# Kernel optimization log

Measured on AMD Instinct MI355X. Metric: run time of the kernel, lower is better.

Reference implementation:

```python
import jax, jax.numpy as jnp
import numpy as np

HEADS = 8

def setup_inputs() -> dict:
    key = jax.random.key(0)
    ks = jax.random.split(key, 5)
    B, C, H, W = 2, 256, 64, 64
    dim = C
    x = jax.random.normal(ks[0], (B, C, H, W), dtype=jnp.float32)
    # Linear weights stored as [in, out] so y = x @ W + b
    w_qkv = jax.random.normal(ks[1], (dim, 3 * dim), dtype=jnp.float32) * (dim ** -0.5)
    b_qkv = jax.random.normal(ks[2], (3 * dim,), dtype=jnp.float32) * 0.02
    w_out = jax.random.normal(ks[3], (dim, dim), dtype=jnp.float32) * (dim ** -0.5)
    b_out = jax.random.normal(ks[4], (dim,), dtype=jnp.float32) * 0.02
    return {"x": x, "w_qkv": w_qkv, "b_qkv": b_qkv, "w_out": w_out, "b_out": b_out}

def reference(x, w_qkv, b_qkv, w_out, b_out):
    B, C, H, W = x.shape
    h = HEADS
    d = C // h
    scale = d ** -0.5
    # [B, C, H, W] -> [B, N, C]
    tokens = x.reshape(B, C, H * W).transpose(0, 2, 1)
    qkv = tokens @ w_qkv + b_qkv  # [B, N, 3C]
    q, k, v = jnp.split(qkv, 3, axis=-1)
    def to_heads(t):
        Bn, N, _ = t.shape
        return t.reshape(Bn, N, h, d).transpose(0, 2, 1, 3)  # [B, h, N, d]
    q, k, v = map(to_heads, (q, k, v))
    dots = jnp.einsum('bhnd,bhmd->bhnm', q, k) * scale  # [B, h, N, N]
    attn = jax.nn.softmax(dots, axis=-1)
    out = jnp.einsum('bhnm,bhmd->bhnd', attn, v)  # [B, h, N, d]
    out = out.transpose(0, 2, 1, 3).reshape(B, H * W, C)  # [B, N, C]
    out = out @ w_out + b_out
    return out.transpose(0, 2, 1).reshape(B, C, H, W)
```

## Files before the change

### kernel.cpp

```cpp
#include <hip/hip_runtime.h>

typedef __attribute__((ext_vector_type(8))) short s16x8;
typedef __attribute__((ext_vector_type(4))) float f32x4;
typedef __attribute__((ext_vector_type(16))) float f32x16;
typedef __attribute__((ext_vector_type(2))) unsigned u32x2;
typedef __attribute__((ext_vector_type(4))) unsigned u32x4;

#define MFMA32(a, b, c) __builtin_amdgcn_mfma_f32_16x16x32_bf16((a), (b), (c), 0, 0, 0)

#if __has_builtin(__builtin_amdgcn_mfma_f32_32x32x16_bf16)
#define MFMA3216(a, b, c) __builtin_amdgcn_mfma_f32_32x32x16_bf16((a), (b), (c), 0, 0, 0)
#else
#define MFMA3216(a, b, c) (c)
#endif

#if __has_builtin(__builtin_amdgcn_exp2f)
#define EXP2F(x) __builtin_amdgcn_exp2f(x)
#else
#define EXP2F(x) __exp2f(x)
#endif

#if __has_builtin(__builtin_amdgcn_rcpf)
#define RCPF(x) __builtin_amdgcn_rcpf(x)
#else
#define RCPF(x) (1.0f / (x))
#endif

#define SL2E 0.25507313f

__device__ __forceinline__ unsigned pkrne(float a, float b) {
  unsigned ua = __builtin_bit_cast(unsigned, a);
  unsigned ub = __builtin_bit_cast(unsigned, b);
  ua += 0x7FFFu + ((ua >> 16) & 1u);
  ub += 0x7FFFu + ((ub >> 16) & 1u);
  return __builtin_amdgcn_perm(ub, ua, 0x07060302u);
}

__device__ __forceinline__ unsigned pktrunc(float a, float b) {
  return __builtin_amdgcn_perm(__builtin_bit_cast(unsigned, b),
                               __builtin_bit_cast(unsigned, a), 0x07060302u);
}

__device__ __forceinline__ unsigned short bfr(float f) {
  unsigned u = __builtin_bit_cast(unsigned, f);
  u += 0x7FFFu + ((u >> 16) & 1u);
  return (unsigned short)(u >> 16);
}

__device__ __forceinline__ float bflo(unsigned u) {
  return __builtin_bit_cast(float, u << 16);
}
__device__ __forceinline__ float bfhi(unsigned u) {
  return __builtin_bit_cast(float, u & 0xFFFF0000u);
}

__device__ __forceinline__ u32x2 plswap(unsigned a, unsigned b) {
#if __has_builtin(__builtin_amdgcn_permlane32_swap)
  return __builtin_amdgcn_permlane32_swap(a, b, false, false);
#else
  unsigned sa = (unsigned)__shfl_xor((int)a, 32, 64);
  unsigned sb = (unsigned)__shfl_xor((int)b, 32, 64);
  bool hi = (threadIdx.x & 63) >= 32;
  u32x2 r;
  r.x = hi ? sb : a;
  r.y = hi ? b : sa;
  return r;
#endif
}

__device__ __forceinline__ void stage16(const ushort* g, ushort* l, int lane) {
#if __has_builtin(__builtin_amdgcn_global_load_lds)
  __builtin_amdgcn_global_load_lds(
      (__attribute__((address_space(1))) unsigned int*)(unsigned long long)(
          const void*)g,
      (__attribute__((address_space(3))) unsigned int*)(unsigned)(
          unsigned long long)(const void*)l,
      16, 0, 0);
#else
  *(uint4*)(l + lane * 8) = *(const uint4*)g;
#endif
}

__device__ __forceinline__ size_t flX(int n, int k) {
  return (size_t)(n >> 7) * 32768 + (size_t)(k >> 5) * 4096 +
         ((n >> 4) & 7) * 512 + ((k >> 3) & 3) * 128 + (n & 15) * 8 + (k & 7);
}
__device__ __forceinline__ size_t flW(int n, int k) {
  return (size_t)(n >> 6) * 16384 + (size_t)(k >> 5) * 2048 +
         ((n >> 4) & 3) * 512 + ((k >> 3) & 3) * 128 + (n & 15) * 8 + (k & 7);
}

__global__ __launch_bounds__(256) void prep_kernel(
    const float* __restrict__ x, const float* __restrict__ wqkv,
    const float* __restrict__ wout, ushort* __restrict__ xbf,
    ushort* __restrict__ wT, ushort* __restrict__ woT) {
  const int t = threadIdx.x;
  const int sub = t & 15, grp = t >> 4;
  const int id = blockIdx.x;
  const float* src;
  ushort* dst;
  int src_ld, k0, n0;
  bool isX = false;
  float sc = 1.f;
  if (id < 512) {
    int mt = id & 63, kt = (id >> 6) & 3, b = id >> 8;
    src = x + (size_t)b * 256 * 4096;
    src_ld = 4096;
    dst = xbf + (size_t)b * 1048576;
    k0 = kt * 64;
    n0 = mt * 64;
    isX = true;
  } else if (id < 560) {
    int r = id - 512, nt = r % 12, kt = r / 12;
    src = wqkv;
    src_ld = 768;
    dst = wT;
    k0 = kt * 64;
    n0 = nt * 64;
    if (n0 < 256) sc = SL2E;
  } else {
    int r = id - 560, nt = r & 3, kt = r >> 2;
    src = wout;
    src_ld = 256;
    dst = woT;
    k0 = kt * 64;
    n0 = nt * 64;
  }
  const int k = k0 + grp * 4;
  const int n = n0 + sub * 4;
  unsigned d0[4], d1[4];
#pragma unroll
  for (int i = 0; i < 4; ++i) {
    float4 v = *(const float4*)(src + (size_t)(k + i) * src_ld + n);
    d0[i] = pkrne(v.x * sc, v.y * sc);
    d1[i] = pkrne(v.z * sc, v.w * sc);
  }
  u32x2 r0 = {__builtin_amdgcn_perm(d0[1], d0[0], 0x05040100u),
              __builtin_amdgcn_perm(d0[3], d0[2], 0x05040100u)};
  u32x2 r1 = {__builtin_amdgcn_perm(d0[1], d0[0], 0x07060302u),
              __builtin_amdgcn_perm(d0[3], d0[2], 0x07060302u)};
  u32x2 r2 = {__builtin_amdgcn_perm(d1[1], d1[0], 0x05040100u),
              __builtin_amdgcn_perm(d1[3], d1[2], 0x05040100u)};
  u32x2 r3 = {__builtin_amdgcn_perm(d1[1], d1[0], 0x07060302u),
              __builtin_amdgcn_perm(d1[3], d1[2], 0x07060302u)};
  if (isX) {
    *(u32x2*)(dst + flX(n + 0, k)) = r0;
    *(u32x2*)(dst + flX(n + 1, k)) = r1;
    *(u32x2*)(dst + flX(n + 2, k)) = r2;
    *(u32x2*)(dst + flX(n + 3, k)) = r3;
  } else {
    *(u32x2*)(dst + flW(n + 0, k)) = r0;
    *(u32x2*)(dst + flW(n + 1, k)) = r1;
    *(u32x2*)(dst + flW(n + 2, k)) = r2;
    *(u32x2*)(dst + flW(n + 3, k)) = r3;
  }
}

__global__ __launch_bounds__(256) void qkv_kernel(
    const ushort* __restrict__ xbf, const ushort* __restrict__ wT,
    const float* __restrict__ bq, ushort* __restrict__ QG,
    ushort* __restrict__ KG, ushort* __restrict__ VtG) {
  __shared__ __align__(64) ushort WL[2][2048];
  __shared__ __align__(64) ushort XL[2][4096];
  const int t0 = blockIdx.x * 128;
  const int n0 = blockIdx.y * 64;
  const int t = threadIdx.x;
  const int wid = t >> 6, lane = t & 63;
  const int wy = wid >> 1, wx = wid & 1;
  const int quad = lane >> 4, l16 = lane & 15;
  const int lo8 = lane * 8;
  f32x4 acc[2][4] = {};
  const ushort* wsrc = wT + (size_t)blockIdx.y * 16384 + wid * 512 + lo8;
  const ushort* xsrc = xbf + (size_t)blockIdx.x * 32768 + wid * 1024 + lo8;
  stage16(wsrc, &WL[0][wid * 512], lane);
  stage16(xsrc, &XL[0][wid * 1024], lane);
  stage16(xsrc + 512, &XL[0][wid * 1024 + 512], lane);
  __syncthreads();
#pragma unroll
  for (int ks = 0; ks < 8; ++ks) {
    const int cur = ks & 1;
    if (ks + 1 < 8) {
      stage16(wsrc + (ks + 1) * 2048, &WL[cur ^ 1][wid * 512], lane);
      stage16(xsrc + (size_t)(ks + 1) * 4096, &XL[cur ^ 1][wid * 1024], lane);
      stage16(xsrc + (size_t)(ks + 1) * 4096 + 512,
              &XL[cur ^ 1][wid * 1024 + 512], lane);
    }
    s16x8 wf[2], xf[4];
#pragma unroll
    for (int i = 0; i < 2; ++i)
      wf[i] = *(const s16x8*)&WL[cur][(2 * wy + i) * 512 + lo8];
#pragma unroll
    for (int j = 0; j < 4; ++j)
      xf[j] = *(const s16x8*)&XL[cur][(4 * wx + j) * 512 + lo8];
#pragma unroll
    for (int i = 0; i < 2; ++i)
#pragma unroll
      for (int j = 0; j < 4; ++j) acc[i][j] = MFMA32(wf[i], xf[j], acc[i][j]);
    __syncthreads();
  }
  if (n0 < 256) {
#pragma unroll
    for (int i = 0; i < 2; ++i) {
      int nb = n0 + 32 * wy + 16 * i + 4 * quad;
      float4 b4 = *(const float4*)(bq + nb);
      float bx0 = b4.x * SL2E, bx1 = b4.y * SL2E, bx2 = b4.z * SL2E,
            bx3 = b4.w * SL2E;
      int h = ((nb & 255) >> 5);
      int dd0 = nb & 31;
#pragma unroll
      for (int j = 0; j < 4; ++j) {
        int tok = t0 + 64 * wx + 16 * j + l16;
        int b = tok >> 12, tokn = tok & 4095;
        u32x2 pk = {pkrne(acc[i][j][0] + bx0, acc[i][j][1] + bx1),
                    pkrne(acc[i][j][2] + bx2, acc[i][j][3] + bx3)};
        *(u32x2*)(QG + ((size_t)(b * 8 + h) * 4096 + tokn) * 32 + dd0) = pk;
      }
    }
  } else if (n0 < 512) {
#pragma unroll
    for (int i = 0; i < 2; ++i) {
      int nb = n0 + 32 * wy + 16 * i + 4 * quad;
      float4 b4 = *(const float4*)(bq + nb);
      float bx0 = b4.x, bx1 = b4.y, bx2 = b4.z, bx3 = b4.w;
      int h = ((nb & 255) >> 5);
      size_t fo = (size_t)i * 512 + (quad >> 1) * 256 + (quad & 1) * 4;
#pragma unroll
      for (int j = 0; j < 4; ++j) {
        int tok = t0 + 64 * wx + 16 * j + l16;
        int b = tok >> 12, tokn = tok & 4095;
        int tl = tokn >> 6, ss = (tokn >> 5) & 1, l5 = tokn & 31;
        u32x2 pk = {pkrne(acc[i][j][0] + bx0, acc[i][j][1] + bx1),
                    pkrne(acc[i][j][2] + bx2, acc[i][j][3] + bx3)};
        *(u32x2*)(KG + (size_t)(b * 8 + h) * 131072 + (size_t)tl * 2048 +
                  ss * 1024 + l5 * 8 + fo) = pk;
      }
    }
  } else {
#pragma unroll
    for (int i = 0; i < 2; ++i) {
      int nb = n0 + 32 * wy + 16 * i + 4 * quad;
      float4 b4 = *(const float4*)(bq + nb);
      float bb[4] = {b4.x, b4.y, b4.z, b4.w};
#pragma unroll
      for (int r = 0; r < 4; ++r) {
        int nn = nb + r - 512;
        int h = nn >> 5, d = nn & 31;
#pragma unroll
        for (int j = 0; j < 4; ++j) {
          int tok = t0 + 64 * wx + 16 * j + l16;
          int b = tok >> 12, tokn = tok & 4095;
          int tl = tokn >> 6, ss = (tokn >> 5) & 1;
          int hV = (tokn >> 4) & 1, hii = (tokn >> 3) & 1, e = tokn & 7;
          VtG[(size_t)(b * 8 + h) * 131072 + (size_t)tl * 2048 + ss * 1024 +
              hV * 512 + hii * 256 + d * 8 + e] = bfr(acc[i][j][r] + bb[r]);
        }
      }
    }
  }
}

__device__ __forceinline__ void softpv(const f32x16& S, s16x8 va0, s16x8 va1,
                                       f32x16& o, f32x16& o_l) {
  const s16x8 ones8 = {(short)0x3F80, (short)0x3F80, (short)0x3F80,
                       (short)0x3F80, (short)0x3F80, (short)0x3F80,
                       (short)0x3F80, (short)0x3F80};
  unsigned w8[8];
#pragma unroll
  for (int ii = 0; ii < 8; ++ii)
    w8[ii] = pktrunc(EXP2F(S[2 * ii]), EXP2F(S[2 * ii + 1]));
  u32x2 sw0 = plswap(w8[0], w8[2]);
  u32x2 sw1 = plswap(w8[1], w8[3]);
  u32x2 sw2 = plswap(w8[4], w8[6]);
  u32x2 sw3 = plswap(w8[5], w8[7]);
  u32x4 pa0 = {sw0.x, sw1.x, sw0.y, sw1.y};
  u32x4 pa1 = {sw2.x, sw3.x, sw2.y, sw3.y};
  const s16x8 pA0 = __builtin_bit_cast(s16x8, pa0);
  const s16x8 pA1 = __builtin_bit_cast(s16x8, pa1);
  o = MFMA3216(pA0, va0, o);
  o = MFMA3216(pA1, va1, o);
  o_l = MFMA3216(pA0, ones8, o_l);
  o_l = MFMA3216(pA1, ones8, o_l);
}

#define ATILE(BUF, KOFF, VOFF)                                              \
  {                                                                         \
    const ushort* kb = &KVs[BUF][KOFF];                                     \
    const ushort* vb = &KVs[BUF][VOFF];                                     \
    f32x16 S0 = MFMA3216(*(const s16x8*)(kb + lo8), qf0, fz);               \
    S0 = MFMA3216(*(const s16x8*)(kb + 512 + lo8), qf1, S0);                \
    softpv(S0, *(const s16x8*)(vb + lo8), *(const s16x8*)(vb + 512 + lo8),  \
           o, o_l);                                                         \
    f32x16 S1 = MFMA3216(*(const s16x8*)(kb + 1024 + lo8), qf0, fz);        \
    S1 = MFMA3216(*(const s16x8*)(kb + 1536 + lo8), qf1, S1);               \
    softpv(S1, *(const s16x8*)(vb + 1024 + lo8),                            \
           *(const s16x8*)(vb + 1536 + lo8), o, o_l);                       \
  }

#define ASTAGE(BUF)                                    \
  {                                                    \
    stage16(kpre, &KVs[BUF][kdst], lane);              \
    stage16(kpre + 2048, &KVs[BUF][2048 + kdst], lane); \
    stage16(vpre, &KVs[BUF][4096 + kdst], lane);       \
    stage16(vpre + 2048, &KVs[BUF][6144 + kdst], lane); \
    kpre += 4096;                                      \
    vpre += 4096;                                      \
  }

__global__ __launch_bounds__(256, 4) void attn_split(
    const ushort* __restrict__ QG, const ushort* __restrict__ KG,
    const ushort* __restrict__ VtG, ushort* __restrict__ OF0,
    ushort* __restrict__ OFb, float* __restrict__ LF) {
  __shared__ __align__(64) ushort KVs[2][8192];
  const int id = blockIdx.x;
  const int bh = (id & 7) * 2 + ((id >> 3) & 1);
  const int q0 = ((id >> 4) & 31) * 128;
  const int sp = id >> 9;
  const int kt0 = sp * 32;
  const int t = threadIdx.x;
  const int wid = t >> 6, lane = t & 63;
  const int l5 = lane & 31, hi = lane >> 5;
  const int lo8 = lane * 8;
  const ushort* qp = QG + (size_t)bh * 4096 * 32;
  const int qw = q0 + 32 * wid;
  const ushort* qrow = qp + (size_t)(qw + l5) * 32 + hi * 8;
  const s16x8 qf0 = *(const s16x8*)(qrow);
  const s16x8 qf1 = *(const s16x8*)(qrow + 16);
  const int kdst = wid * 512;
  const ushort* kpre =
      KG + (size_t)bh * 131072 + (size_t)kt0 * 2048 + kdst + lo8;
  const ushort* vpre =
      VtG + (size_t)bh * 131072 + (size_t)kt0 * 2048 + kdst + lo8;
  ASTAGE(0)
  __syncthreads();
  f32x16 o = {};
  f32x16 o_l = {};
  const f32x16 fz = {};
  for (int p = 0; p < 8; ++p) {
    ASTAGE(1)
    ATILE(0, 0, 4096)
    ATILE(0, 2048, 6144)
    __syncthreads();
    if (p < 7) {
      ASTAGE(0)
    }
    ATILE(1, 0, 4096)
    ATILE(1, 2048, 6144)
    __syncthreads();
  }
  ushort* OFs = (sp == 0) ? OF0 : OFb;
  float* LFs = LF + (size_t)sp * 65536;
#pragma unroll
  for (int r = 0; r < 16; ++r) {
    int q = qw + (r & 3) + 8 * (r >> 2) + 4 * hi;
    OFs[((size_t)bh * 4096 + q) * 32 + l5] = bfr(o[r]);
  }
  float lval = o_l[0];
#pragma unroll
  for (int r = 1; r < 16; ++r) lval = (l5 == r) ? o_l[r] : lval;
  if (l5 < 16)
    LFs[(size_t)bh * 4096 + qw + (l5 & 3) + 8 * (l5 >> 2) + 4 * hi] = lval;
}

__global__ __launch_bounds__(256) void proj_split(
    const ushort* __restrict__ OF0, const ushort* __restrict__ OFb,
    const float* __restrict__ LF, const ushort* __restrict__ woT,
    const float* __restrict__ bo, float* __restrict__ out) {
  __shared__ __align__(64) ushort WL[2048];
  __shared__ __align__(16) ushort Xl[64][40];
  const int t0 = blockIdx.x * 64;
  const int c0 = blockIdx.y * 64;
  const int t = threadIdx.x;
  const int wid = t >> 6, lane = t & 63;
  const int wy = wid >> 1, wx = wid & 1;
  const int quad = lane >> 4, l16 = lane & 15;
  const int lo8 = lane * 8;
  f32x4 acc[2][2] = {};
  const int c8 = (t & 7) * 4;
  const ushort* wsrc = woT + (size_t)blockIdx.y * 16384 + wid * 512 + lo8;
  for (int k0 = 0; k0 < 256; k0 += 32) {
    __syncthreads();
    stage16(wsrc + (k0 >> 5) * 2048, &WL[wid * 512], lane);
    const int hh = k0 >> 5;
#pragma unroll
    for (int p = 0; p < 2; ++p) {
      int row = 32 * p + (t >> 3);
      int tok = t0 + row, bb = tok >> 12, tokn = tok & 4095;
      size_t ro = (size_t)(bb * 8 + hh) * 4096 + tokn;
      size_t oi = ro * 32 + c8;
      uint2 a0 = *(const uint2*)(OF0 + oi);
      uint2 a1 = *(const uint2*)(OFb + oi);
      float l = LF[ro] + LF[65536 + ro];
      float inv = RCPF(l);
      f32x4 s;
      s[0] = bflo(a0.x) + bflo(a1.x);
      s[1] = bfhi(a0.x) + bfhi(a1.x);
      s[2] = bflo(a0.y) + bflo(a1.y);
      s[3] = bfhi(a0.y) + bfhi(a1.y);
      s *= inv;
      u32x2 pk = {pkrne(s[0], s[1]), pkrne(s[2], s[3])};
      *(u32x2*)&Xl[row][c8] = pk;
    }
    __syncthreads();
    s16x8 wf[2], xf[2];
#pragma unroll
    for (int i = 0; i < 2; ++i)
      wf[i] = *(const s16x8*)&WL[(2 * wy + i) * 512 + lo8];
#pragma unroll
    for (int j = 0; j < 2; ++j)
      xf[j] = *(const s16x8*)&Xl[32 * wx + 16 * j + l16][quad * 8];
#pragma unroll
    for (int i = 0; i < 2; ++i)
#pragma unroll
      for (int j = 0; j < 2; ++j) acc[i][j] = MFMA32(wf[i], xf[j], acc[i][j]);
  }
#pragma unroll
  for (int i = 0; i < 2; ++i) {
    int cb = c0 + 32 * wy + 16 * i + 4 * quad;
    float4 b4 = *(const float4*)(bo + cb);
    float bb[4] = {b4.x, b4.y, b4.z, b4.w};
#pragma unroll
    for (int j = 0; j < 2; ++j) {
      int tok = t0 + 32 * wx + 16 * j + l16;
      int b = tok >> 12, tokn = tok & 4095;
#pragma unroll
      for (int r = 0; r < 4; ++r)
        out[((size_t)(b * 256 + cb + r)) * 4096 + tokn] = acc[i][j][r] + bb[r];
    }
  }
}

extern "C" void kernel_launch(void* const* d_in, const int* in_sizes, int n_in,
                              void* d_out, int out_size, void* d_ws, size_t ws_size,
                              hipStream_t stream) {
  (void)in_sizes; (void)n_in; (void)out_size; (void)ws_size;
  const float* x = (const float*)d_in[0];
  const float* wq = (const float*)d_in[1];
  const float* bq = (const float*)d_in[2];
  const float* wo = (const float*)d_in[3];
  const float* bo = (const float*)d_in[4];
  float* out = (float*)d_out;
  ushort* ws = (ushort*)d_ws;
  ushort* xbf = ws;
  ushort* OF0 = ws;
  ushort* QG  = ws + 2097152;
  ushort* KG  = ws + 4194304;
  ushort* VtG = ws + 6291456;
  ushort* wT  = ws + 8388608;
  ushort* woT = ws + 8585216;
  ushort* OFb = ws + 8650752;
  float* LF = (float*)(ws + 12845056);
  prep_kernel<<<576, 256, 0, stream>>>(x, wq, wo, xbf, wT, woT);
  qkv_kernel<<<dim3(64, 12), 256, 0, stream>>>(xbf, wT, bq, QG, KG, VtG);
  attn_split<<<1024, 256, 0, stream>>>(QG, KG, VtG, OF0, OFb, LF);
  proj_split<<<dim3(128, 4), 256, 0, stream>>>(OF0, OFb, LF, woT, bo, out);
}
```

Baseline: 135.4 us.

## Fuse fp32-to-bf16 conversion into QKV GEMM and fold wout prep into attention

Removes the separate prep kernel. The QKV GEMM now reads fp32 x and w_qkv directly. Each block converts its 64x256 weight slice to bf16 into LDS, and converts x tiles from an fp32 LDS buffer while forming the MFMA fragments. The w_out transpose and conversion run as 16 extra blocks appended to the attention launch. This saves one launch and the xbf/wT round trips through global memory. In exchange, every QKV block redoes the weight conversion, the x loads are no longer double-buffered, and the k-loop has two barriers per iteration.

Result: slower. 148.3 us (+9.6%).

```diff
diff --git a/kernel.cpp b/kernel.cpp
--- a/kernel.cpp
+++ b/kernel.cpp
@@ -81,87 +81,17 @@
 #endif
 }
 
-__device__ __forceinline__ size_t flX(int n, int k) {
-  return (size_t)(n >> 7) * 32768 + (size_t)(k >> 5) * 4096 +
-         ((n >> 4) & 7) * 512 + ((k >> 3) & 3) * 128 + (n & 15) * 8 + (k & 7);
-}
 __device__ __forceinline__ size_t flW(int n, int k) {
   return (size_t)(n >> 6) * 16384 + (size_t)(k >> 5) * 2048 +
          ((n >> 4) & 3) * 512 + ((k >> 3) & 3) * 128 + (n & 15) * 8 + (k & 7);
 }
 
-__global__ __launch_bounds__(256) void prep_kernel(
+__global__ __launch_bounds__(256) void qkv_fused(
     const float* __restrict__ x, const float* __restrict__ wqkv,
-    const float* __restrict__ wout, ushort* __restrict__ xbf,
-    ushort* __restrict__ wT, ushort* __restrict__ woT) {
-  const int t = threadIdx.x;
-  const int sub = t & 15, grp = t >> 4;
-  const int id = blockIdx.x;
-  const float* src;
-  ushort* dst;
-  int src_ld, k0, n0;
-  bool isX = false;
-  float sc = 1.f;
-  if (id < 512) {
-    int mt = id & 63, kt = (id >> 6) & 3, b = id >> 8;
-    src = x + (size_t)b * 256 * 4096;
-    src_ld = 4096;
-    dst = xbf + (size_t)b * 1048576;
-    k0 = kt * 64;
-    n0 = mt * 64;
-    isX = true;
-  } else if (id < 560) {
-    int r = id - 512, nt = r % 12, kt = r / 12;
-    src = wqkv;
-    src_ld = 768;
-    dst = wT;
-    k0 = kt * 64;
-    n0 = nt * 64;
-    if (n0 < 256) sc = SL2E;
-  } else {
-    int r = id - 560, nt = r & 3, kt = r >> 2;
-    src = wout;
-    src_ld = 256;
-    dst = woT;
-    k0 = kt * 64;
-    n0 = nt * 64;
-  }
-  const int k = k0 + grp * 4;
-  const int n = n0 + sub * 4;
-  unsigned d0[4], d1[4];
-#pragma unroll
-  for (int i = 0; i < 4; ++i) {
-    float4 v = *(const float4*)(src + (size_t)(k + i) * src_ld + n);
-    d0[i] = pkrne(v.x * sc, v.y * sc);
-    d1[i] = pkrne(v.z * sc, v.w * sc);
-  }
-  u32x2 r0 = {__builtin_amdgcn_perm(d0[1], d0[0], 0x05040100u),
-              __builtin_amdgcn_perm(d0[3], d0[2], 0x05040100u)};
-  u32x2 r1 = {__builtin_amdgcn_perm(d0[1], d0[0], 0x07060302u),
-              __builtin_amdgcn_perm(d0[3], d0[2], 0x07060302u)};
-  u32x2 r2 = {__builtin_amdgcn_perm(d1[1], d1[0], 0x05040100u),
-              __builtin_amdgcn_perm(d1[3], d1[2], 0x05040100u)};
-  u32x2 r3 = {__builtin_amdgcn_perm(d1[1], d1[0], 0x07060302u),
-              __builtin_amdgcn_perm(d1[3], d1[2], 0x07060302u)};
-  if (isX) {
-    *(u32x2*)(dst + flX(n + 0, k)) = r0;
-    *(u32x2*)(dst + flX(n + 1, k)) = r1;
-    *(u32x2*)(dst + flX(n + 2, k)) = r2;
-    *(u32x2*)(dst + flX(n + 3, k)) = r3;
-  } else {
-    *(u32x2*)(dst + flW(n + 0, k)) = r0;
-    *(u32x2*)(dst + flW(n + 1, k)) = r1;
-    *(u32x2*)(dst + flW(n + 2, k)) = r2;
-    *(u32x2*)(dst + flW(n + 3, k)) = r3;
-  }
-}
-
-__global__ __launch_bounds__(256) void qkv_kernel(
-    const ushort* __restrict__ xbf, const ushort* __restrict__ wT,
     const float* __restrict__ bq, ushort* __restrict__ QG,
     ushort* __restrict__ KG, ushort* __restrict__ VtG) {
-  __shared__ __align__(64) ushort WL[2][2048];
-  __shared__ __align__(64) ushort XL[2][4096];
+  __shared__ __align__(16) ushort WF[16384];
+  __shared__ __align__(16) float XF[32][133];
   const int t0 = blockIdx.x * 128;
   const int n0 = blockIdx.y * 64;
   const int t = threadIdx.x;
@@ -169,34 +99,67 @@
   const int wy = wid >> 1, wx = wid & 1;
   const int quad = lane >> 4, l16 = lane & 15;
   const int lo8 = lane * 8;
+  const float sc = (n0 < 256) ? SL2E : 1.f;
+  const int sub = t & 15, grp = t >> 4;
+  {
+    const int nl = sub * 4;
+#pragma unroll
+    for (int kt = 0; kt < 4; ++kt) {
+      const int k = kt * 64 + grp * 4;
+      unsigned d0[4], d1[4];
+#pragma unroll
+      for (int i = 0; i < 4; ++i) {
+        float4 v = *(const float4*)(wqkv + (size_t)(k + i) * 768 + n0 + nl);
+        d0[i] = pkrne(v.x * sc, v.y * sc);
+        d1[i] = pkrne(v.z * sc, v.w * sc);
+      }
+      u32x2 r0 = {__builtin_amdgcn_perm(d0[1], d0[0], 0x05040100u),
+                  __builtin_amdgcn_perm(d0[3], d0[2], 0x05040100u)};
+      u32x2 r1 = {__builtin_amdgcn_perm(d0[1], d0[0], 0x07060302u),
+                  __builtin_amdgcn_perm(d0[3], d0[2], 0x07060302u)};
+      u32x2 r2 = {__builtin_amdgcn_perm(d1[1], d1[0], 0x05040100u),
+                  __builtin_amdgcn_perm(d1[3], d1[2], 0x05040100u)};
+      u32x2 r3 = {__builtin_amdgcn_perm(d1[1], d1[0], 0x07060302u),
+                  __builtin_amdgcn_perm(d1[3], d1[2], 0x07060302u)};
+      const int ks = k >> 5, kq = (k >> 3) & 3, ke = k & 7;
+      ushort* wbase = WF + ks * 2048 + kq * 128 + ke;
+      *(u32x2*)(wbase + ((nl + 0) >> 4) * 512 + ((nl + 0) & 15) * 8) = r0;
+      *(u32x2*)(wbase + ((nl + 1) >> 4) * 512 + ((nl + 1) & 15) * 8) = r1;
+      *(u32x2*)(wbase + ((nl + 2) >> 4) * 512 + ((nl + 2) & 15) * 8) = r2;
+      *(u32x2*)(wbase + ((nl + 3) >> 4) * 512 + ((nl + 3) & 15) * 8) = r3;
+    }
+  }
+  const int bb = t0 >> 12, tokn0 = t0 & 4095;
+  const float* xb = x + (size_t)bb * 1048576 + tokn0;
+  const int xr = t >> 3, xc = (t & 7) * 16;
   f32x4 acc[2][4] = {};
-  const ushort* wsrc = wT + (size_t)blockIdx.y * 16384 + wid * 512 + lo8;
-  const ushort* xsrc = xbf + (size_t)blockIdx.x * 32768 + wid * 1024 + lo8;
-  stage16(wsrc, &WL[0][wid * 512], lane);
-  stage16(xsrc, &XL[0][wid * 1024], lane);
-  stage16(xsrc + 512, &XL[0][wid * 1024 + 512], lane);
-  __syncthreads();
-#pragma unroll
   for (int ks = 0; ks < 8; ++ks) {
-    const int cur = ks & 1;
-    if (ks + 1 < 8) {
-      stage16(wsrc + (ks + 1) * 2048, &WL[cur ^ 1][wid * 512], lane);
-      stage16(xsrc + (size_t)(ks + 1) * 4096, &XL[cur ^ 1][wid * 1024], lane);
-      stage16(xsrc + (size_t)(ks + 1) * 4096 + 512,
-              &XL[cur ^ 1][wid * 1024 + 512], lane);
-    }
+    __syncthreads();
+#pragma unroll
+    for (int u = 0; u < 4; ++u) {
+      float4 v =
+          *(const float4*)(xb + (size_t)(ks * 32 + xr) * 4096 + xc + u * 4);
+      *(float4*)&XF[xr][xc + u * 4] = v;
+    }
+    __syncthreads();
     s16x8 wf[2], xf[4];
 #pragma unroll
     for (int i = 0; i < 2; ++i)
-      wf[i] = *(const s16x8*)&WL[cur][(2 * wy + i) * 512 + lo8];
-#pragma unroll
-    for (int j = 0; j < 4; ++j)
-      xf[j] = *(const s16x8*)&XL[cur][(4 * wx + j) * 512 + lo8];
+      wf[i] = *(const s16x8*)&WF[ks * 2048 + (2 * wy + i) * 512 + lo8];
+#pragma unroll
+    for (int j = 0; j < 4; ++j) {
+      const int tl = 64 * wx + 16 * j + l16;
+      const int kk = quad * 8;
+      u32x4 px = {pkrne(XF[kk + 0][tl], XF[kk + 1][tl]),
+                  pkrne(XF[kk + 2][tl], XF[kk + 3][tl]),
+                  pkrne(XF[kk + 4][tl], XF[kk + 5][tl]),
+                  pkrne(XF[kk + 6][tl], XF[kk + 7][tl])};
+      xf[j] = __builtin_bit_cast(s16x8, px);
+    }
 #pragma unroll
     for (int i = 0; i < 2; ++i)
 #pragma unroll
       for (int j = 0; j < 4; ++j) acc[i][j] = MFMA32(wf[i], xf[j], acc[i][j]);
-    __syncthreads();
   }
   if (n0 < 256) {
 #pragma unroll
@@ -240,7 +203,7 @@
     for (int i = 0; i < 2; ++i) {
       int nb = n0 + 32 * wy + 16 * i + 4 * quad;
       float4 b4 = *(const float4*)(bq + nb);
-      float bb[4] = {b4.x, b4.y, b4.z, b4.w};
+      float bb4[4] = {b4.x, b4.y, b4.z, b4.w};
 #pragma unroll
       for (int r = 0; r < 4; ++r) {
         int nn = nb + r - 512;
@@ -252,7 +215,7 @@
           int tl = tokn >> 6, ss = (tokn >> 5) & 1;
           int hV = (tokn >> 4) & 1, hii = (tokn >> 3) & 1, e = tokn & 7;
           VtG[(size_t)(b * 8 + h) * 131072 + (size_t)tl * 2048 + ss * 1024 +
-              hV * 512 + hii * 256 + d * 8 + e] = bfr(acc[i][j][r] + bb[r]);
+              hV * 512 + hii * 256 + d * 8 + e] = bfr(acc[i][j][r] + bb4[r]);
         }
       }
     }
@@ -296,27 +259,55 @@
            *(const s16x8*)(vb + 1536 + lo8), o, o_l);                       \
   }
 
-#define ASTAGE(BUF)                                    \
-  {                                                    \
-    stage16(kpre, &KVs[BUF][kdst], lane);              \
+#define ASTAGE(BUF)                                     \
+  {                                                     \
+    stage16(kpre, &KVs[BUF][kdst], lane);               \
     stage16(kpre + 2048, &KVs[BUF][2048 + kdst], lane); \
-    stage16(vpre, &KVs[BUF][4096 + kdst], lane);       \
+    stage16(vpre, &KVs[BUF][4096 + kdst], lane);        \
     stage16(vpre + 2048, &KVs[BUF][6144 + kdst], lane); \
-    kpre += 4096;                                      \
-    vpre += 4096;                                      \
+    kpre += 4096;                                       \
+    vpre += 4096;                                       \
   }
 
 __global__ __launch_bounds__(256, 4) void attn_split(
     const ushort* __restrict__ QG, const ushort* __restrict__ KG,
     const ushort* __restrict__ VtG, ushort* __restrict__ OF0,
-    ushort* __restrict__ OFb, float* __restrict__ LF) {
+    ushort* __restrict__ OFb, float* __restrict__ LF,
+    const float* __restrict__ wo, ushort* __restrict__ woT) {
   __shared__ __align__(64) ushort KVs[2][8192];
   const int id = blockIdx.x;
+  const int t = threadIdx.x;
+  if (id >= 1024) {
+    const int r = id - 1024;
+    const int nt = r & 3, kt = r >> 2;
+    const int sub = t & 15, grp = t >> 4;
+    const int k = kt * 64 + grp * 4;
+    const int n = nt * 64 + sub * 4;
+    unsigned d0[4], d1[4];
+#pragma unroll
+    for (int i = 0; i < 4; ++i) {
+      float4 v = *(const float4*)(wo + (size_t)(k + i) * 256 + n);
+      d0[i] = pkrne(v.x, v.y);
+      d1[i] = pkrne(v.z, v.w);
+    }
+    u32x2 r0 = {__builtin_amdgcn_perm(d0[1], d0[0], 0x05040100u),
+                __builtin_amdgcn_perm(d0[3], d0[2], 0x05040100u)};
+    u32x2 r1 = {__builtin_amdgcn_perm(d0[1], d0[0], 0x07060302u),
+                __builtin_amdgcn_perm(d0[3], d0[2], 0x07060302u)};
+    u32x2 r2 = {__builtin_amdgcn_perm(d1[1], d1[0], 0x05040100u),
+                __builtin_amdgcn_perm(d1[3], d1[2], 0x05040100u)};
+    u32x2 r3 = {__builtin_amdgcn_perm(d1[1], d1[0], 0x07060302u),
+                __builtin_amdgcn_perm(d1[3], d1[2], 0x07060302u)};
+    *(u32x2*)(woT + flW(n + 0, k)) = r0;
+    *(u32x2*)(woT + flW(n + 1, k)) = r1;
+    *(u32x2*)(woT + flW(n + 2, k)) = r2;
+    *(u32x2*)(woT + flW(n + 3, k)) = r3;
+    return;
+  }
   const int bh = (id & 7) * 2 + ((id >> 3) & 1);
   const int q0 = ((id >> 4) & 31) * 128;
   const int sp = id >> 9;
   const int kt0 = sp * 32;
-  const int t = threadIdx.x;
   const int wid = t >> 6, lane = t & 63;
   const int l5 = lane & 31, hi = lane >> 5;
   const int lo8 = lane * 8;
@@ -440,17 +431,14 @@
   const float* bo = (const float*)d_in[4];
   float* out = (float*)d_out;
   ushort* ws = (ushort*)d_ws;
-  ushort* xbf = ws;
   ushort* OF0 = ws;
   ushort* QG  = ws + 2097152;
   ushort* KG  = ws + 4194304;
   ushort* VtG = ws + 6291456;
-  ushort* wT  = ws + 8388608;
   ushort* woT = ws + 8585216;
   ushort* OFb = ws + 8650752;
   float* LF = (float*)(ws + 12845056);
-  prep_kernel<<<576, 256, 0, stream>>>(x, wq, wo, xbf, wT, woT);
-  qkv_kernel<<<dim3(64, 12), 256, 0, stream>>>(xbf, wT, bq, QG, KG, VtG);
-  attn_split<<<1024, 256, 0, stream>>>(QG, KG, VtG, OF0, OFb, LF);
+  qkv_fused<<<dim3(64, 12), 256, 0, stream>>>(x, wq, bq, QG, KG, VtG);
+  attn_split<<<1040, 256, 0, stream>>>(QG, KG, VtG, OF0, OFb, LF, wo, woT);
   proj_split<<<dim3(128, 4), 256, 0, stream>>>(OF0, OFb, LF, woT, bo, out);
 }
```

## Split attention KV range four ways across two launches

Applied to the files above, without the earlier changes.

The attention kernel now handles a quarter of the key range per block instead of half. It is launched twice with a base offset, producing four partial outputs and four row-sum buffers. The projection kernel then sums all four partials before normalizing. The intent is to shorten each block's serial loop and expose more parallelism. The cost is an extra launch and extra global traffic for the partial outputs. Workspace buffers are relocated, and wT now aliases OF1, which is safe only because wT is consumed before attention writes OF1.

After: 137.8 us. No clear change (+1.8%).

```diff
diff --git a/kernel.cpp b/kernel.cpp
--- a/kernel.cpp
+++ b/kernel.cpp
@@ -296,26 +296,26 @@
            *(const s16x8*)(vb + 1536 + lo8), o, o_l);                       \
   }
 
-#define ASTAGE(BUF)                                    \
-  {                                                    \
-    stage16(kpre, &KVs[BUF][kdst], lane);              \
+#define ASTAGE(BUF)                                     \
+  {                                                     \
+    stage16(kpre, &KVs[BUF][kdst], lane);               \
     stage16(kpre + 2048, &KVs[BUF][2048 + kdst], lane); \
-    stage16(vpre, &KVs[BUF][4096 + kdst], lane);       \
+    stage16(vpre, &KVs[BUF][4096 + kdst], lane);        \
     stage16(vpre + 2048, &KVs[BUF][6144 + kdst], lane); \
-    kpre += 4096;                                      \
-    vpre += 4096;                                      \
+    kpre += 4096;                                       \
+    vpre += 4096;                                       \
   }
 
 __global__ __launch_bounds__(256, 4) void attn_split(
     const ushort* __restrict__ QG, const ushort* __restrict__ KG,
-    const ushort* __restrict__ VtG, ushort* __restrict__ OF0,
-    ushort* __restrict__ OFb, float* __restrict__ LF) {
+    const ushort* __restrict__ VtG, ushort* __restrict__ OFa,
+    ushort* __restrict__ OFc, float* __restrict__ LFq, int base_q) {
   __shared__ __align__(64) ushort KVs[2][8192];
   const int id = blockIdx.x;
   const int bh = (id & 7) * 2 + ((id >> 3) & 1);
   const int q0 = ((id >> 4) & 31) * 128;
   const int sp = id >> 9;
-  const int kt0 = sp * 32;
+  const int kt0 = (base_q + sp) * 16;
   const int t = threadIdx.x;
   const int wid = t >> 6, lane = t & 63;
   const int l5 = lane & 31, hi = lane >> 5;
@@ -335,20 +335,20 @@
   f32x16 o = {};
   f32x16 o_l = {};
   const f32x16 fz = {};
-  for (int p = 0; p < 8; ++p) {
+  for (int p = 0; p < 4; ++p) {
     ASTAGE(1)
     ATILE(0, 0, 4096)
     ATILE(0, 2048, 6144)
     __syncthreads();
-    if (p < 7) {
+    if (p < 3) {
       ASTAGE(0)
     }
     ATILE(1, 0, 4096)
     ATILE(1, 2048, 6144)
     __syncthreads();
   }
-  ushort* OFs = (sp == 0) ? OF0 : OFb;
-  float* LFs = LF + (size_t)sp * 65536;
+  ushort* OFs = (sp == 0) ? OFa : OFc;
+  float* LFs = LFq + (size_t)sp * 65536;
 #pragma unroll
   for (int r = 0; r < 16; ++r) {
     int q = qw + (r & 3) + 8 * (r >> 2) + 4 * hi;
@@ -362,7 +362,8 @@
 }
 
 __global__ __launch_bounds__(256) void proj_split(
-    const ushort* __restrict__ OF0, const ushort* __restrict__ OFb,
+    const ushort* __restrict__ OF0, const ushort* __restrict__ OF1,
+    const ushort* __restrict__ OF2, const ushort* __restrict__ OF3,
     const float* __restrict__ LF, const ushort* __restrict__ woT,
     const float* __restrict__ bo, float* __restrict__ out) {
   __shared__ __align__(64) ushort WL[2048];
@@ -388,14 +389,16 @@
       size_t ro = (size_t)(bb * 8 + hh) * 4096 + tokn;
       size_t oi = ro * 32 + c8;
       uint2 a0 = *(const uint2*)(OF0 + oi);
-      uint2 a1 = *(const uint2*)(OFb + oi);
-      float l = LF[ro] + LF[65536 + ro];
+      uint2 a1 = *(const uint2*)(OF1 + oi);
+      uint2 a2 = *(const uint2*)(OF2 + oi);
+      uint2 a3 = *(const uint2*)(OF3 + oi);
+      float l = LF[ro] + LF[65536 + ro] + LF[131072 + ro] + LF[196608 + ro];
       float inv = RCPF(l);
       f32x4 s;
-      s[0] = bflo(a0.x) + bflo(a1.x);
-      s[1] = bfhi(a0.x) + bfhi(a1.x);
-      s[2] = bflo(a0.y) + bflo(a1.y);
-      s[3] = bfhi(a0.y) + bfhi(a1.y);
+      s[0] = bflo(a0.x) + bflo(a1.x) + bflo(a2.x) + bflo(a3.x);
+      s[1] = bfhi(a0.x) + bfhi(a1.x) + bfhi(a2.x) + bfhi(a3.x);
+      s[2] = bflo(a0.y) + bflo(a1.y) + bflo(a2.y) + bflo(a3.y);
+      s[3] = bfhi(a0.y) + bfhi(a1.y) + bfhi(a2.y) + bfhi(a3.y);
       s *= inv;
       u32x2 pk = {pkrne(s[0], s[1]), pkrne(s[2], s[3])};
       *(u32x2*)&Xl[row][c8] = pk;
@@ -445,12 +448,16 @@
   ushort* QG  = ws + 2097152;
   ushort* KG  = ws + 4194304;
   ushort* VtG = ws + 6291456;
-  ushort* wT  = ws + 8388608;
-  ushort* woT = ws + 8585216;
-  ushort* OFb = ws + 8650752;
-  float* LF = (float*)(ws + 12845056);
+  float*  LF  = (float*)(ws + 8388608);
+  ushort* woT = ws + 8912896;
+  ushort* wT  = ws + 8978432;
+  ushort* OF1 = ws + 8978432;
+  ushort* OF2 = ws + 11075584;
+  ushort* OF3 = ws + 13172736;
   prep_kernel<<<576, 256, 0, stream>>>(x, wq, wo, xbf, wT, woT);
   qkv_kernel<<<dim3(64, 12), 256, 0, stream>>>(xbf, wT, bq, QG, KG, VtG);
-  attn_split<<<1024, 256, 0, stream>>>(QG, KG, VtG, OF0, OFb, LF);
-  proj_split<<<dim3(128, 4), 256, 0, stream>>>(OF0, OFb, LF, woT, bo, out);
-}
+  attn_split<<<1024, 256, 0, stream>>>(QG, KG, VtG, OF0, OF1, LF, 0);
+  attn_split<<<1024, 256, 0, stream>>>(QG, KG, VtG, OF2, OF3, LF + 131072, 2);
+  proj_split<<<dim3(128, 4), 256, 0, stream>>>(OF0, OF1, OF2, OF3, LF, woT,
+                                               bo, out);
+}
```
